# Kernel optimization log

Hardware: AMD Instinct MI355X
Metric: run time of the kernel (lower is better)

## Reference

```python
import jax, jax.numpy as jnp
import numpy as np

B, T, H, K = 128, 32, 256, 32


def setup_inputs() -> dict:
    key = jax.random.key(0)
    ks = jax.random.split(key, 24)
    s = 0.02  # small weight scale keeps exp(pdf) stable

    def n(k, shape, scale=s):
        return jax.random.normal(k, shape, dtype=jnp.float32) * scale

    inp = {
        "input_encoded": jax.random.normal(ks[0], (B, T, H), dtype=jnp.float32),
        "y_prev": jax.random.normal(ks[1], (B, T), dtype=jnp.float32),
        "attn_W1": n(ks[2], (H, 3 * H)),
        "attn_b1": n(ks[3], (H,)),
        "attn_W2": n(ks[4], (1, H)),
        "attn_b2": n(ks[5], (1,)),
        "fc_W": n(ks[6], (1, H + 1)),
        "fc_b": n(ks[7], (1,)),
        "var_W": n(ks[8], (H, H + 1)),
        "var_b": n(ks[9], (H,)),
        "W_ih": n(ks[10], (4 * H, 1)),
        "W_hh": n(ks[11], (4 * H, H)),
        "b_ih": n(ks[12], (4 * H,)),
        "b_hh": n(ks[13], (4 * H,)),
        "fc_dec_W": n(ks[14], (1, H)),
        "fc_dec_b": n(ks[15], (1,)),
        "pdf_W": n(ks[16], (1, H + 1)),
        "pdf_b": n(ks[17], (1,)),
        "fc_enc_W": n(ks[18], (1, H)),
        "fc_enc_b": n(ks[19], (1,)),
        "num_particles": K,
    }
    return inp


def reference(input_encoded, y_prev, attn_W1, attn_b1, attn_W2, attn_b2,
              fc_W, fc_b, var_W, var_b, W_ih, W_hh, b_ih, b_hh,
              fc_dec_W, fc_dec_b, pdf_W, pdf_b, fc_enc_W, fc_enc_b,
              num_particles):
    Bn, Tn, Hn = input_encoded.shape
    Kn = num_particles
    base = jax.random.key(42)
    arB = jnp.arange(Bn)

    def step(carry, xs):
        hiddens, cells = carry  # each (K*B, H), flat index = k*B + b
        t, y_t = xs  # y_t: (B,)
        k1, k2 = jax.random.split(jax.random.fold_in(base, t))
        # particle means (torch: mean over dim 0 of (K, B, H) view)
        hm = hiddens.reshape(Kn, Bn, Hn).mean(axis=0)  # (B, H)
        cm = cells.reshape(Kn, Bn, Hn).mean(axis=0)
        # attention over encoder timesteps
        x = jnp.concatenate([
            jnp.broadcast_to(hm[:, None, :], (Bn, Tn, Hn)),
            jnp.broadcast_to(cm[:, None, :], (Bn, Tn, Hn)),
            input_encoded], axis=2)  # (B, T, 3H)
        a = jnp.tanh(x @ attn_W1.T + attn_b1) @ attn_W2.T + attn_b2  # (B, T, 1)
        beta = jax.nn.softmax(a[..., 0], axis=1)  # (B, T)
        context = jnp.einsum('bt,bth->bh', beta, input_encoded)  # (B, H)
        y_tilde = jnp.concatenate([context, y_t[:, None]], axis=1) @ fc_W.T + fc_b  # (B, 1)
        var = jnp.concatenate([y_tilde, hm], axis=1) @ var_W.T + var_b  # (B, H)
        # single-step LSTM cell over all particles (torch gate order i,f,g,o)
        x_in = jnp.tile(y_tilde, (Kn, 1))  # (K*B, 1)
        gates = x_in @ W_ih.T + b_ih + hiddens @ W_hh.T + b_hh  # (K*B, 4H)
        i, f, g, o = jnp.split(gates, 4, axis=1)
        c_new = jax.nn.sigmoid(f) * cells + jax.nn.sigmoid(i) * jnp.tanh(g)
        h_new = jax.nn.sigmoid(o) * jnp.tanh(c_new)
        # reparameterization: h = mu + eps * softplus(var)
        std = jnp.tile(jax.nn.softplus(var), (Kn, 1))  # (K*B, H)
        eps = jax.random.normal(k1, (Kn * Bn, Hn), dtype=h_new.dtype)
        h_new = h_new + eps * std
        # sort_hidden: per-batch argsort of 1-d projection, gather hiddens only
        proj = h_new @ fc_dec_W.T + fc_dec_b  # (K*B, 1)
        idx = jnp.argsort(proj.reshape(Kn, Bn).T, axis=1)  # (B, K)
        flat = (arB[:, None] + idx * Bn).T.reshape(-1)  # (K*B,)
        h_sorted = h_new[flat]
        # particle weights (replicates torch's view(-1, K, 1) reshape exactly)
        y = jnp.concatenate([h_sorted, jnp.tile(y_tilde, (Kn, 1))], axis=1)
        prob = jnp.exp(y @ pdf_W.T + pdf_b).reshape(Bn, Kn, 1)
        prob = prob / prob.sum(axis=1, keepdims=True)
        # soft-resampling: multinomial over (B, K) rows (torch: prob.view(K,-1).T)
        logits = jnp.log(prob.reshape(Kn, Bn).T)  # (B, K)
        samp = jax.random.categorical(k2, logits, shape=(Kn, Bn))  # (K, B)
        flat2 = (samp * Bn + arB[None, :]).reshape(-1)
        return (h_sorted[flat2], c_new[flat2]), context

    h0 = jnp.zeros((Kn * Bn, Hn), dtype=input_encoded.dtype)
    (hiddens, _), contexts = jax.lax.scan(step, (h0, h0), (jnp.arange(Tn), y_prev.T))
    context = contexts[-1]
    hm = hiddens.reshape(Kn, Bn, Hn).mean(axis=0)  # (B, H)
    y_pred = hm @ fc_dec_W.T + fc_dec_b + context @ fc_enc_W.T + fc_enc_b  # (B, 1)
    return y_pred
```

## Files before the change

### kernel.cpp

```cpp
#include <hip/hip_runtime.h>
#include <cstdint>


#define Bn 128
#define Tn 32
#define Hn 256
#define Kn 32

__host__ __device__ inline void tf2x32(uint32_t k0, uint32_t k1, uint32_t x0, uint32_t x1,
                                       uint32_t &o0, uint32_t &o1) {
  uint32_t ks2 = k0 ^ k1 ^ 0x1BD11BDAu;
  x0 += k0; x1 += k1;
#define TFR(r) { x0 += x1; x1 = (x1 << r) | (x1 >> (32 - r)); x1 ^= x0; }
  TFR(13) TFR(15) TFR(26) TFR(6)
  x0 += k1;  x1 += ks2 + 1u;
  TFR(17) TFR(29) TFR(16) TFR(24)
  x0 += ks2; x1 += k0 + 2u;
  TFR(13) TFR(15) TFR(26) TFR(6)
  x0 += k0;  x1 += k1 + 3u;
  TFR(17) TFR(29) TFR(16) TFR(24)
  x0 += k1;  x1 += ks2 + 4u;
  TFR(13) TFR(15) TFR(26) TFR(6)
  x0 += ks2; x1 += k0 + 5u;
#undef TFR
  o0 = x0; o1 = x1;
}

__device__ __forceinline__ float erfinv_xla(float x) {
  float w = -log1pf(-x * x);
  float p;
  if (w < 5.0f) {
    w = w - 2.5f;
    p = 2.81022636e-08f;
    p = fmaf(p, w, 3.43273939e-07f);
    p = fmaf(p, w, -3.5233877e-06f);
    p = fmaf(p, w, -4.39150654e-06f);
    p = fmaf(p, w, 0.00021858087f);
    p = fmaf(p, w, -0.00125372503f);
    p = fmaf(p, w, -0.00417768164f);
    p = fmaf(p, w, 0.246640727f);
    p = fmaf(p, w, 1.50140941f);
  } else {
    w = sqrtf(w) - 3.0f;
    p = -0.000200214257f;
    p = fmaf(p, w, 0.000100950558f);
    p = fmaf(p, w, 0.00134934322f);
    p = fmaf(p, w, -0.00367342844f);
    p = fmaf(p, w, 0.00573950773f);
    p = fmaf(p, w, -0.0076224613f);
    p = fmaf(p, w, 0.00943887047f);
    p = fmaf(p, w, 1.00167406f);
    p = fmaf(p, w, 2.83297682f);
  }
  return p * x;
}

__device__ __forceinline__ float sigmoid_xla(float x) {
  return 0.5f + 0.5f * tanhf(0.5f * x);
}

__device__ __forceinline__ float u01_from_bits(uint32_t bits) {
  return __uint_as_float((bits >> 9) | 0x3F800000u) - 1.0f;
}

__device__ __forceinline__ float normal_from_idx(uint32_t ka, uint32_t kb, uint32_t idx) {
  uint32_t o0, o1; tf2x32(ka, kb, 0u, idx, o0, o1);
  float f = u01_from_bits(o0 ^ o1);
  const float LO = __uint_as_float(0xBF7FFFFFu);
  float u = fmaxf(LO, f * 2.0f + LO);
  return __uint_as_float(0x3FB504F3u) * erfinv_xla(u);
}

__device__ __forceinline__ float gumbel_from_idx(uint32_t ka, uint32_t kb, uint32_t idx) {
  uint32_t o0, o1; tf2x32(ka, kb, 0u, idx, o0, o1);
  float f = u01_from_bits(o0 ^ o1);
  const float TINY = __uint_as_float(0x00800000u);
  float u = fmaxf(TINY, f + TINY);
  return -logf(-logf(u));
}


__global__ void darnn_p0(const float* __restrict__ W1, const float* __restrict__ Whh,
                         const float* __restrict__ varW,
                         float* __restrict__ W1hT, float* __restrict__ W1cT,
                         float* __restrict__ W1eT, float* __restrict__ WhhT,
                         float* __restrict__ varWT) {
  int bid = blockIdx.x, tid = threadIdx.x;
  if (bid < 768) {
    int part = bid >> 8, j = bid & 255;
    float v = W1[tid * 768 + part * 256 + j];
    float* dst = (part == 0) ? W1hT : (part == 1) ? W1cT : W1eT;
    dst[j * 256 + tid] = v;
  } else if (bid < 1024) {
    int j = bid - 768;
    for (int idx = tid; idx < 1024; idx += 256) {
      int h = idx >> 2, q = idx & 3;
      WhhT[j * 1024 + idx] = Whh[(q * 256 + h) * 256 + j];
    }
  } else {
    int j2 = bid - 1024;
    varWT[j2 * 256 + tid] = varW[tid * 257 + j2];
  }
}

__global__ void darnn_p1(const float* __restrict__ enc, const float* __restrict__ W1eT,
                         const float* __restrict__ b1, float* __restrict__ encW1) {
  int bt = blockIdx.x, tid = threadIdx.x;
  __shared__ float se[256];
  se[tid] = enc[bt * 256 + tid];
  __syncthreads();
  float acc = 0.f;
  for (int j = 0; j < 256; ++j) acc = fmaf(se[j], W1eT[j * 256 + tid], acc);
  encW1[bt * 256 + tid] = acc + b1[tid];
}


__launch_bounds__(1024, 4)
__global__ void darnn_step(const float* __restrict__ enc, const float* __restrict__ yprev,
                           const float* __restrict__ W1hT, const float* __restrict__ W1cT,
                           const float* __restrict__ encW1, const float* __restrict__ W2,
                           const float* __restrict__ b2p, const float* __restrict__ fcW,
                           const float* __restrict__ fcbp, const float* __restrict__ varWT,
                           const float* __restrict__ varb, const float* __restrict__ WhhT,
                           const float* __restrict__ Wih, const float* __restrict__ bih,
                           const float* __restrict__ bhh, const float* __restrict__ decW,
                           const float* __restrict__ decbp, const float* __restrict__ pdfW,
                           const float* __restrict__ pdfbp,
                           const float* __restrict__ proj_p, const float* __restrict__ pdot_p,
                           const float* __restrict__ ytl_p,
                           const float* __restrict__ hprev, const float* __restrict__ cprev,
                           float* __restrict__ hcur, float* __restrict__ ccur,
                           float* __restrict__ proj_c, float* __restrict__ pdot_c,
                           float* __restrict__ ytl_c, float* __restrict__ ctx_g,
                           int t, uint32_t k1a, uint32_t k1b, uint32_t k2a, uint32_t k2b) {
  const int bid = blockIdx.x, tid = threadIdx.x;
  const int b = bid & 127, khalf = bid >> 7;
  const int bg = b >> 5, bloc = b & 31;
  const int h = tid & 255, kg = tid >> 8, lane = tid & 63;

  __shared__ __align__(16) float s_h[32 * 256];
  __shared__ float s_gp[1024], s_w[1024];
  __shared__ int s_srck[1024];
  __shared__ float s_ytlp[32], s_den[32], s_logit[32];
  __shared__ int s_rowH[32], s_rowC[32];
  __shared__ float s_hm[256], s_cm[256], s_hmc[256], s_red[256], s_std[256];
  __shared__ float s_sc[32], s_beta[32];
  __shared__ float s_ytl;
  __shared__ float s_sredP[16 * 4], s_sredQ[16 * 4];

  if (t > 0) {
    if (tid < 32) s_ytlp[tid] = ytl_p[bg * 32 + tid];
    {
      int bl = tid >> 5, k = tid & 31;
      s_gp[tid] = proj_p[k * 128 + bg * 32 + bl];
    }
    __syncthreads();
    {
      int bl = tid >> 5, k = tid & 31;
      float p = s_gp[tid];
      const float* gp = s_gp + bl * 32;
      int rank = 0;
      for (int kk = 0; kk < 32; ++kk) {
        float q = gp[kk];
        rank += (q < p) || (q == p && kk < k);
      }
      s_srck[bl * 32 + rank] = k;
      float wv = expf((pdot_p[k * 128 + bg * 32 + bl] + s_ytlp[bl] * pdfW[256]) + pdfbp[0]);
      s_w[bl * 32 + rank] = wv;
    }
    __syncthreads();
    if (tid < 32) {
      float s = 0.f;
      for (int bl = 0; bl < 32; ++bl) s += s_w[bl * 32 + tid];
      s_den[tid] = s;
    }
    __syncthreads();
    if (tid < 32) s_logit[tid] = logf(s_w[bloc * 32 + tid] / s_den[tid]);
    __syncthreads();
    if (tid < 32) {
      int ko = tid, r2 = ko * 128 + b;
      float best = gumbel_from_idx(k2a, k2b, (uint32_t)(r2 * 32)) + s_logit[0];
      int sv = 0;
      for (int k = 1; k < 32; ++k) {
        float v = gumbel_from_idx(k2a, k2b, (uint32_t)(r2 * 32 + k)) + s_logit[k];
        if (v > best) { best = v; sv = k; }
      }
      s_rowH[ko] = s_srck[bloc * 32 + sv] * 128 + b;
      s_rowC[ko] = sv * 128 + b;
    }
  } else {
    if (tid < 32) {
      s_rowH[tid] = tid * 128 + b;
      s_rowC[tid] = tid * 128 + b;
    }
  }
  __syncthreads();

  {
    const float4* hp = (const float4*)hprev;
    float4* sh4 = (float4*)s_h;
#pragma unroll
    for (int ii = 0; ii < 2; ++ii) {
      int i = tid + ii * 1024;
      int rr = i >> 6, c4 = i & 63;
      sh4[i] = hp[(size_t)s_rowH[rr] * 64 + c4];
    }
  }
  __syncthreads();

  if (tid < 256) {
    float s1 = 0.f;
    for (int k = 0; k < 32; ++k) s1 += s_h[k * 256 + tid];
    s_hm[tid] = s1 * 0.03125f;
  } else if (tid < 512) {
    int j = tid & 255;
    float s2 = 0.f;
    for (int k = 0; k < 32; ++k) s2 += cprev[(size_t)s_rowC[k] * 256 + j];
    s_cm[j] = s2 * 0.03125f;
  }
  __syncthreads();
  if (tid < 256) {
    float acc = 0.f;
    for (int j = 0; j < 256; ++j) {
      acc = fmaf(s_hm[j], W1hT[j * 256 + tid], acc);
      acc = fmaf(s_cm[j], W1cT[j * 256 + tid], acc);
    }
    s_hmc[tid] = acc;
  }
  __syncthreads();
  {
    int wv = tid >> 6;
    for (int tt = wv * 2; tt < wv * 2 + 2; ++tt) {
      float p = 0.f;
      for (int hh = lane; hh < 256; hh += 64)
        p += tanhf(encW1[(b * 32 + tt) * 256 + hh] + s_hmc[hh]) * W2[hh];
      for (int off = 32; off; off >>= 1) p += __shfl_down(p, off);
      if (lane == 0) s_sc[tt] = p + b2p[0];
    }
  }
  __syncthreads();
  if (tid == 0) {
    float m = s_sc[0];
    for (int k = 1; k < 32; ++k) m = fmaxf(m, s_sc[k]);
    float s = 0.f;
    for (int k = 0; k < 32; ++k) { float e = expf(s_sc[k] - m); s_beta[k] = e; s += e; }
    for (int k = 0; k < 32; ++k) s_beta[k] /= s;
  }
  __syncthreads();
  if (tid < 256) {
    float cx = 0.f;
    for (int tt = 0; tt < 32; ++tt) cx = fmaf(s_beta[tt], enc[(b * 32 + tt) * 256 + tid], cx);
    if (khalf == 0) ctx_g[b * 256 + tid] = cx;
    s_red[tid] = cx * fcW[tid];
  }
  __syncthreads();
  if (tid == 0) {
    float s = 0.f;
    for (int j = 0; j < 256; ++j) s += s_red[j];
    s += yprev[b * 32 + t] * fcW[256];
    s_ytl = s + fcbp[0];
    if (khalf == 0) ytl_c[b] = s_ytl;
  }
  __syncthreads();
  if (tid < 256) {
    float v = s_ytl * varWT[tid];
    for (int j = 0; j < 256; ++j) v = fmaf(s_hm[j], varWT[(1 + j) * 256 + tid], v);
    v += varb[tid];
    s_std[tid] = fmaxf(v, 0.f) + log1pf(expf(-fabsf(v)));
  }
  __syncthreads();

  float ai[4], af[4], ag[4], ao[4];
#pragma unroll
  for (int r = 0; r < 4; ++r) { ai[r] = af[r] = ag[r] = ao[r] = 0.f; }
  {
    const float4* wp = (const float4*)WhhT + h;
    const float* shr = s_h + (khalf * 16 + kg * 4) * 256;
    float4 wa0 = wp[0 * 256], wa1 = wp[1 * 256], wa2 = wp[2 * 256], wa3 = wp[3 * 256];
    for (int j = 0; j < 256; j += 4) {
      int jn = (j + 4) & 255;
      float4 wb0 = wp[(jn + 0) * 256];
      float4 wb1 = wp[(jn + 1) * 256];
      float4 wb2 = wp[(jn + 2) * 256];
      float4 wb3 = wp[(jn + 3) * 256];
#pragma unroll
      for (int r = 0; r < 4; ++r) {
        float4 h4 = *(const float4*)(shr + r * 256 + j);
        ai[r] = fmaf(h4.x, wa0.x, ai[r]); ai[r] = fmaf(h4.y, wa1.x, ai[r]);
        ai[r] = fmaf(h4.z, wa2.x, ai[r]); ai[r] = fmaf(h4.w, wa3.x, ai[r]);
        af[r] = fmaf(h4.x, wa0.y, af[r]); af[r] = fmaf(h4.y, wa1.y, af[r]);
        af[r] = fmaf(h4.z, wa2.y, af[r]); af[r] = fmaf(h4.w, wa3.y, af[r]);
        ag[r] = fmaf(h4.x, wa0.z, ag[r]); ag[r] = fmaf(h4.y, wa1.z, ag[r]);
        ag[r] = fmaf(h4.z, wa2.z, ag[r]); ag[r] = fmaf(h4.w, wa3.z, ag[r]);
        ao[r] = fmaf(h4.x, wa0.w, ao[r]); ao[r] = fmaf(h4.y, wa1.w, ao[r]);
        ao[r] = fmaf(h4.z, wa2.w, ao[r]); ao[r] = fmaf(h4.w, wa3.w, ao[r]);
      }
      wa0 = wb0; wa1 = wb1; wa2 = wb2; wa3 = wb3;
    }
  }

  const float bI = bih[h], bF = bih[256 + h], bG = bih[512 + h], bO = bih[768 + h];
  const float dI = bhh[h], dF = bhh[256 + h], dG = bhh[512 + h], dO = bhh[768 + h];
  const float wI = Wih[h], wF = Wih[256 + h], wG = Wih[512 + h], wO = Wih[768 + h];
  float hnv[4];
#pragma unroll
  for (int r = 0; r < 4; ++r) {
    int rl = kg * 4 + r;
    int k = khalf * 16 + rl, R = k * 128 + b;
    float xb = s_ytl;
    float pi = ((xb * wI + bI) + ai[r]) + dI;
    float pf = ((xb * wF + bF) + af[r]) + dF;
    float pg = ((xb * wG + bG) + ag[r]) + dG;
    float po = ((xb * wO + bO) + ao[r]) + dO;
    float c_old = cprev[(size_t)s_rowC[k] * 256 + h];
    float cn = sigmoid_xla(pf) * c_old + sigmoid_xla(pi) * tanhf(pg);
    float hn = sigmoid_xla(po) * tanhf(cn);
    float eps = normal_from_idx(k1a, k1b, (uint32_t)(R * 256 + h));
    hn = hn + eps * s_std[h];
    ccur[(size_t)R * 256 + h] = cn;
    hcur[(size_t)R * 256 + h] = hn;
    hnv[r] = hn;
  }

  const float dw = decW[h], pw = pdfW[h];
#pragma unroll
  for (int r = 0; r < 4; ++r) {
    int rl = kg * 4 + r;
    float v = hnv[r] * dw;
    for (int off = 32; off; off >>= 1) v += __shfl_down(v, off);
    if (lane == 0) s_sredP[rl * 4 + (h >> 6)] = v;
    float v2 = hnv[r] * pw;
    for (int off = 32; off; off >>= 1) v2 += __shfl_down(v2, off);
    if (lane == 0) s_sredQ[rl * 4 + (h >> 6)] = v2;
  }
  __syncthreads();
  if (tid < 16) {
    int rl = tid, k = khalf * 16 + rl;
    proj_c[k * 128 + b] = ((s_sredP[rl * 4 + 0] + s_sredP[rl * 4 + 1]) +
                           (s_sredP[rl * 4 + 2] + s_sredP[rl * 4 + 3])) + decbp[0];
  } else if (tid < 32) {
    int rl = tid - 16, k = khalf * 16 + rl;
    pdot_c[k * 128 + b] = (s_sredQ[rl * 4 + 0] + s_sredQ[rl * 4 + 1]) +
                          (s_sredQ[rl * 4 + 2] + s_sredQ[rl * 4 + 3]);
  }
}


__launch_bounds__(256)
__global__ void darnn_kout(const float* __restrict__ proj_g, const float* __restrict__ pdot_g,
                           const float* __restrict__ ytl_prev, const float* __restrict__ hprev,
                           const float* __restrict__ ctx_g, const float* __restrict__ decW,
                           const float* __restrict__ decbp, const float* __restrict__ encWo,
                           const float* __restrict__ encbo, const float* __restrict__ pdfW,
                           const float* __restrict__ pdfbp,
                           uint32_t k2a, uint32_t k2b, float* __restrict__ out) {
  const int b = blockIdx.x, tid = threadIdx.x, bg = b >> 5, bloc = b & 31;
  const int lane = tid & 63;
  __shared__ float s_gp[1024], s_w[1024];
  __shared__ int s_srck[1024];
  __shared__ float s_ytlp[32], s_den[32], s_logit[32];
  __shared__ int s_row[32];
  __shared__ float s_hm[256], s_sred[8];

  if (tid < 32) s_ytlp[tid] = ytl_prev[bg * 32 + tid];
  for (int i = tid; i < 1024; i += 256) {
    int bl = i >> 5, k = i & 31;
    s_gp[i] = proj_g[k * 128 + bg * 32 + bl];
  }
  __syncthreads();
  for (int i = tid; i < 1024; i += 256) {
    int bl = i >> 5, k = i & 31;
    float p = s_gp[i];
    const float* gp = s_gp + bl * 32;
    int rank = 0;
    for (int kk = 0; kk < 32; ++kk) {
      float q = gp[kk];
      rank += (q < p) || (q == p && kk < k);
    }
    s_srck[bl * 32 + rank] = k;
    float wv = expf((pdot_g[k * 128 + bg * 32 + bl] + s_ytlp[bl] * pdfW[256]) + pdfbp[0]);
    s_w[bl * 32 + rank] = wv;
  }
  __syncthreads();
  if (tid < 32) {
    float s = 0.f;
    for (int bl = 0; bl < 32; ++bl) s += s_w[bl * 32 + tid];
    s_den[tid] = s;
  }
  __syncthreads();
  if (tid < 32) s_logit[tid] = logf(s_w[bloc * 32 + tid] / s_den[tid]);
  __syncthreads();
  if (tid < 32) {
    int ko = tid, r2 = ko * 128 + b;
    float best = gumbel_from_idx(k2a, k2b, (uint32_t)(r2 * 32)) + s_logit[0];
    int sv = 0;
    for (int k = 1; k < 32; ++k) {
      float v = gumbel_from_idx(k2a, k2b, (uint32_t)(r2 * 32 + k)) + s_logit[k];
      if (v > best) { best = v; sv = k; }
    }
    s_row[ko] = s_srck[bloc * 32 + sv] * 128 + b;
  }
  __syncthreads();
  {
    float s1 = 0.f;
    for (int k = 0; k < 32; ++k) s1 += hprev[(size_t)s_row[k] * 256 + tid];
    s_hm[tid] = s1 * 0.03125f;
  }
  __syncthreads();
  {
    int wvi = tid >> 6;
    float v1 = s_hm[tid] * decW[tid];
    float v2 = ctx_g[b * 256 + tid] * encWo[tid];
    for (int off = 32; off; off >>= 1) { v1 += __shfl_down(v1, off); v2 += __shfl_down(v2, off); }
    if (lane == 0) { s_sred[wvi] = v1; s_sred[4 + wvi] = v2; }
  }
  __syncthreads();
  if (tid == 0) {
    float d1 = (s_sred[0] + s_sred[1]) + (s_sred[2] + s_sred[3]);
    float d2 = (s_sred[4] + s_sred[5]) + (s_sred[6] + s_sred[7]);
    out[b] = ((d1 + decbp[0]) + d2) + encbo[0];
  }
}

extern "C" void kernel_launch(void* const* d_in, const int* in_sizes, int n_in,
                              void* d_out, int out_size, void* d_ws, size_t ws_size,
                              hipStream_t stream) {
  const float* enc   = (const float*)d_in[0];
  const float* yprev = (const float*)d_in[1];
  const float* W1    = (const float*)d_in[2];
  const float* b1    = (const float*)d_in[3];
  const float* W2    = (const float*)d_in[4];
  const float* b2    = (const float*)d_in[5];
  const float* fcW   = (const float*)d_in[6];
  const float* fcb   = (const float*)d_in[7];
  const float* varW  = (const float*)d_in[8];
  const float* varb  = (const float*)d_in[9];
  const float* Wih   = (const float*)d_in[10];
  const float* Whh   = (const float*)d_in[11];
  const float* bih   = (const float*)d_in[12];
  const float* bhh   = (const float*)d_in[13];
  const float* decW  = (const float*)d_in[14];
  const float* decb  = (const float*)d_in[15];
  const float* pdfW  = (const float*)d_in[16];
  const float* pdfb  = (const float*)d_in[17];
  const float* encWo = (const float*)d_in[18];
  const float* encbo = (const float*)d_in[19];

  float* ws = (float*)d_ws;
  size_t o = 0;
  float* encW1 = ws + o; o += (size_t)Bn * Tn * Hn;
  float* W1hT  = ws + o; o += (size_t)Hn * Hn;
  float* W1cT  = ws + o; o += (size_t)Hn * Hn;
  float* W1eT  = ws + o; o += (size_t)Hn * Hn;
  float* WhhT  = ws + o; o += (size_t)Hn * 4 * Hn;
  float* varWT = ws + o; o += (size_t)257 * Hn;
  float* hbuf0 = ws + o; o += (size_t)Kn * Bn * Hn;
  float* hbuf1 = ws + o; o += (size_t)Kn * Bn * Hn;
  float* cbuf0 = ws + o; o += (size_t)Kn * Bn * Hn;
  float* cbuf1 = ws + o; o += (size_t)Kn * Bn * Hn;
  float* ytl0  = ws + o; o += 128;
  float* ytl1  = ws + o; o += 128;
  float* ctx_g = ws + o; o += (size_t)Bn * Hn;
  float* proj0 = ws + o; o += 4096;
  float* proj1 = ws + o; o += 4096;
  float* pdot0 = ws + o; o += 4096;
  float* pdot1 = ws + o; o += 4096;
  if (ws_size < o * sizeof(float)) return;

  float* hb[2] = { hbuf0, hbuf1 };
  float* cb[2] = { cbuf0, cbuf1 };
  float* yb[2] = { ytl0, ytl1 };
  float* pp[2] = { proj0, proj1 };
  float* pq[2] = { pdot0, pdot1 };

  hipMemsetAsync(hbuf1, 0, (size_t)Kn * Bn * Hn * sizeof(float), stream);
  hipMemsetAsync(cbuf1, 0, (size_t)Kn * Bn * Hn * sizeof(float), stream);

  darnn_p0<<<1281, 256, 0, stream>>>(W1, Whh, varW, W1hT, W1cT, W1eT, WhhT, varWT);
  darnn_p1<<<Bn * Tn, 256, 0, stream>>>(enc, W1eT, b1, encW1);

  uint32_t k2pa = 0, k2pb = 0;
  for (int t = 0; t < Tn; ++t) {
    uint32_t f0, f1, k1a, k1b, k2a, k2b;
    tf2x32(0u, 42u, 0u, (uint32_t)t, f0, f1);
    tf2x32(f0, f1, 0u, 0u, k1a, k1b);
    tf2x32(f0, f1, 0u, 1u, k2a, k2b);
    int cur = t & 1, prv = (t + 1) & 1;

    darnn_step<<<2 * Bn, 1024, 0, stream>>>(enc, yprev, W1hT, W1cT, encW1, W2, b2,
                                            fcW, fcb, varWT, varb, WhhT, Wih, bih, bhh,
                                            decW, decb, pdfW, pdfb,
                                            pp[prv], pq[prv], yb[prv], hb[prv], cb[prv],
                                            hb[cur], cb[cur], pp[cur], pq[cur], yb[cur],
                                            ctx_g, t, k1a, k1b, k2pa, k2pb);
    k2pa = k2a; k2pb = k2b;
  }

  darnn_kout<<<Bn, 256, 0, stream>>>(pp[1], pq[1], yb[1], hb[1], ctx_g,
                                     decW, decb, encWo, encbo, pdfW, pdfb,
                                     k2pa, k2pb, (float*)d_out);
}
```

Measured before the change: 2.866 ms.

## Split particles across four blocks per batch and parallelize Gumbel sampling

The recurrent step kernel now launches four blocks per batch element instead of two, with each block handling 8 particles. This shrinks the shared hidden-state tile and the per-thread gate accumulators, which raises occupancy and parallelism. Gumbel noise for the resampling step is now computed by all 1024 threads into shared memory instead of 32 threads looping serially. The mean and matvec loops are unrolled to batch their global loads, and the first half of the threads computes the means while the rest stage the hidden tile. The cost is that every block repeats the per-batch attention and projection prologue, so that redundant work doubles.

```diff
diff --git a/kernel.cpp b/kernel.cpp
--- a/kernel.cpp
+++ b/kernel.cpp
@@ -115,7 +115,7 @@
 }
 
 
-__launch_bounds__(1024, 4)
+__launch_bounds__(1024, 8)
 __global__ void darnn_step(const float* __restrict__ enc, const float* __restrict__ yprev,
                            const float* __restrict__ W1hT, const float* __restrict__ W1cT,
                            const float* __restrict__ encW1, const float* __restrict__ W2,
@@ -138,15 +138,15 @@
   const int bg = b >> 5, bloc = b & 31;
   const int h = tid & 255, kg = tid >> 8, lane = tid & 63;
 
-  __shared__ __align__(16) float s_h[32 * 256];
-  __shared__ float s_gp[1024], s_w[1024];
+  __shared__ __align__(16) float s_h[8 * 256];
+  __shared__ float s_gp[1024], s_w[1024], s_gvals[1024];
   __shared__ int s_srck[1024];
   __shared__ float s_ytlp[32], s_den[32], s_logit[32];
   __shared__ int s_rowH[32], s_rowC[32];
-  __shared__ float s_hm[256], s_cm[256], s_hmc[256], s_red[256], s_std[256];
+  __shared__ __align__(16) float s_hm[256], s_cm[256], s_hmc[256], s_red[256], s_std[256];
   __shared__ float s_sc[32], s_beta[32];
   __shared__ float s_ytl;
-  __shared__ float s_sredP[16 * 4], s_sredQ[16 * 4];
+  __shared__ float s_sredP[8 * 4], s_sredQ[8 * 4];
 
   if (t > 0) {
     if (tid < 32) s_ytlp[tid] = ytl_p[bg * 32 + tid];
@@ -177,14 +177,17 @@
     __syncthreads();
     if (tid < 32) s_logit[tid] = logf(s_w[bloc * 32 + tid] / s_den[tid]);
     __syncthreads();
+    {
+      int ko = tid >> 5, k = tid & 31, r2 = ko * 128 + b;
+      s_gvals[tid] = gumbel_from_idx(k2a, k2b, (uint32_t)(r2 * 32 + k)) + s_logit[k];
+    }
+    __syncthreads();
     if (tid < 32) {
-      int ko = tid, r2 = ko * 128 + b;
-      float best = gumbel_from_idx(k2a, k2b, (uint32_t)(r2 * 32)) + s_logit[0];
+      int ko = tid;
+      const float* gv = s_gvals + ko * 32;
+      float best = gv[0];
       int sv = 0;
-      for (int k = 1; k < 32; ++k) {
-        float v = gumbel_from_idx(k2a, k2b, (uint32_t)(r2 * 32 + k)) + s_logit[k];
-        if (v > best) { best = v; sv = k; }
-      }
+      for (int k = 1; k < 32; ++k) { float v = gv[k]; if (v > best) { best = v; sv = k; } }
       s_rowH[ko] = s_srck[bloc * 32 + sv] * 128 + b;
       s_rowC[ko] = sv * 128 + b;
     }
@@ -196,38 +199,53 @@
   }
   __syncthreads();
 
-  {
-    const float4* hp = (const float4*)hprev;
-    float4* sh4 = (float4*)s_h;
-#pragma unroll
-    for (int ii = 0; ii < 2; ++ii) {
-      int i = tid + ii * 1024;
-      int rr = i >> 6, c4 = i & 63;
-      sh4[i] = hp[(size_t)s_rowH[rr] * 64 + c4];
-    }
-  }
-  __syncthreads();
-
   if (tid < 256) {
     float s1 = 0.f;
-    for (int k = 0; k < 32; ++k) s1 += s_h[k * 256 + tid];
+    for (int k0 = 0; k0 < 32; k0 += 8) {
+      float hv[8];
+#pragma unroll
+      for (int i = 0; i < 8; ++i) hv[i] = hprev[(size_t)s_rowH[k0 + i] * 256 + tid];
+#pragma unroll
+      for (int i = 0; i < 8; ++i) s1 += hv[i];
+    }
     s_hm[tid] = s1 * 0.03125f;
   } else if (tid < 512) {
     int j = tid & 255;
     float s2 = 0.f;
-    for (int k = 0; k < 32; ++k) s2 += cprev[(size_t)s_rowC[k] * 256 + j];
+    for (int k0 = 0; k0 < 32; k0 += 8) {
+      float cv[8];
+#pragma unroll
+      for (int i = 0; i < 8; ++i) cv[i] = cprev[(size_t)s_rowC[k0 + i] * 256 + j];
+#pragma unroll
+      for (int i = 0; i < 8; ++i) s2 += cv[i];
+    }
     s_cm[j] = s2 * 0.03125f;
-  }
-  __syncthreads();
+  } else {
+    int i = tid - 512;
+    int rr = i >> 6, c4 = i & 63;
+    ((float4*)s_h)[i] = ((const float4*)hprev)[(size_t)s_rowH[khalf * 8 + rr] * 64 + c4];
+  }
+  __syncthreads();
+
   if (tid < 256) {
     float acc = 0.f;
-    for (int j = 0; j < 256; ++j) {
-      acc = fmaf(s_hm[j], W1hT[j * 256 + tid], acc);
-      acc = fmaf(s_cm[j], W1cT[j * 256 + tid], acc);
+    for (int j0 = 0; j0 < 256; j0 += 8) {
+      float wh[8], wc[8];
+#pragma unroll
+      for (int i = 0; i < 8; ++i) {
+        wh[i] = W1hT[(j0 + i) * 256 + tid];
+        wc[i] = W1cT[(j0 + i) * 256 + tid];
+      }
+#pragma unroll
+      for (int i = 0; i < 8; ++i) {
+        acc = fmaf(s_hm[j0 + i], wh[i], acc);
+        acc = fmaf(s_cm[j0 + i], wc[i], acc);
+      }
     }
     s_hmc[tid] = acc;
   }
   __syncthreads();
+
   {
     int wv = tid >> 6;
     for (int tt = wv * 2; tt < wv * 2 + 2; ++tt) {
@@ -255,8 +273,12 @@
   }
   __syncthreads();
   if (tid == 0) {
+    const float4* r4 = (const float4*)s_red;
     float s = 0.f;
-    for (int j = 0; j < 256; ++j) s += s_red[j];
+    for (int i = 0; i < 64; ++i) {
+      float4 v = r4[i];
+      s = s + v.x; s = s + v.y; s = s + v.z; s = s + v.w;
+    }
     s += yprev[b * 32 + t] * fcW[256];
     s_ytl = s + fcbp[0];
     if (khalf == 0) ytl_c[b] = s_ytl;
@@ -264,49 +286,52 @@
   __syncthreads();
   if (tid < 256) {
     float v = s_ytl * varWT[tid];
-    for (int j = 0; j < 256; ++j) v = fmaf(s_hm[j], varWT[(1 + j) * 256 + tid], v);
+    for (int j0 = 0; j0 < 256; j0 += 16) {
+      float wv[16];
+#pragma unroll
+      for (int i = 0; i < 16; ++i) wv[i] = varWT[(1 + j0 + i) * 256 + tid];
+#pragma unroll
+      for (int i = 0; i < 16; ++i) v = fmaf(s_hm[j0 + i], wv[i], v);
+    }
     v += varb[tid];
     s_std[tid] = fmaxf(v, 0.f) + log1pf(expf(-fabsf(v)));
   }
   __syncthreads();
 
-  float ai[4], af[4], ag[4], ao[4];
-#pragma unroll
-  for (int r = 0; r < 4; ++r) { ai[r] = af[r] = ag[r] = ao[r] = 0.f; }
+  float ai[2], af[2], ag[2], ao[2];
+#pragma unroll
+  for (int r = 0; r < 2; ++r) { ai[r] = af[r] = ag[r] = ao[r] = 0.f; }
   {
     const float4* wp = (const float4*)WhhT + h;
-    const float* shr = s_h + (khalf * 16 + kg * 4) * 256;
-    float4 wa0 = wp[0 * 256], wa1 = wp[1 * 256], wa2 = wp[2 * 256], wa3 = wp[3 * 256];
+    const float* shr = s_h + (kg * 2) * 256;
     for (int j = 0; j < 256; j += 4) {
-      int jn = (j + 4) & 255;
-      float4 wb0 = wp[(jn + 0) * 256];
-      float4 wb1 = wp[(jn + 1) * 256];
-      float4 wb2 = wp[(jn + 2) * 256];
-      float4 wb3 = wp[(jn + 3) * 256];
-#pragma unroll
-      for (int r = 0; r < 4; ++r) {
+      float4 w0 = wp[(j + 0) * 256];
+      float4 w1 = wp[(j + 1) * 256];
+      float4 w2 = wp[(j + 2) * 256];
+      float4 w3 = wp[(j + 3) * 256];
+#pragma unroll
+      for (int r = 0; r < 2; ++r) {
         float4 h4 = *(const float4*)(shr + r * 256 + j);
-        ai[r] = fmaf(h4.x, wa0.x, ai[r]); ai[r] = fmaf(h4.y, wa1.x, ai[r]);
-        ai[r] = fmaf(h4.z, wa2.x, ai[r]); ai[r] = fmaf(h4.w, wa3.x, ai[r]);
-        af[r] = fmaf(h4.x, wa0.y, af[r]); af[r] = fmaf(h4.y, wa1.y, af[r]);
-        af[r] = fmaf(h4.z, wa2.y, af[r]); af[r] = fmaf(h4.w, wa3.y, af[r]);
-        ag[r] = fmaf(h4.x, wa0.z, ag[r]); ag[r] = fmaf(h4.y, wa1.z, ag[r]);
-        ag[r] = fmaf(h4.z, wa2.z, ag[r]); ag[r] = fmaf(h4.w, wa3.z, ag[r]);
-        ao[r] = fmaf(h4.x, wa0.w, ao[r]); ao[r] = fmaf(h4.y, wa1.w, ao[r]);
-        ao[r] = fmaf(h4.z, wa2.w, ao[r]); ao[r] = fmaf(h4.w, wa3.w, ao[r]);
+        ai[r] = fmaf(h4.x, w0.x, ai[r]); ai[r] = fmaf(h4.y, w1.x, ai[r]);
+        ai[r] = fmaf(h4.z, w2.x, ai[r]); ai[r] = fmaf(h4.w, w3.x, ai[r]);
+        af[r] = fmaf(h4.x, w0.y, af[r]); af[r] = fmaf(h4.y, w1.y, af[r]);
+        af[r] = fmaf(h4.z, w2.y, af[r]); af[r] = fmaf(h4.w, w3.y, af[r]);
+        ag[r] = fmaf(h4.x, w0.z, ag[r]); ag[r] = fmaf(h4.y, w1.z, ag[r]);
+        ag[r] = fmaf(h4.z, w2.z, ag[r]); ag[r] = fmaf(h4.w, w3.z, ag[r]);
+        ao[r] = fmaf(h4.x, w0.w, ao[r]); ao[r] = fmaf(h4.y, w1.w, ao[r]);
+        ao[r] = fmaf(h4.z, w2.w, ao[r]); ao[r] = fmaf(h4.w, w3.w, ao[r]);
       }
-      wa0 = wb0; wa1 = wb1; wa2 = wb2; wa3 = wb3;
     }
   }
 
   const float bI = bih[h], bF = bih[256 + h], bG = bih[512 + h], bO = bih[768 + h];
   const float dI = bhh[h], dF = bhh[256 + h], dG = bhh[512 + h], dO = bhh[768 + h];
   const float wI = Wih[h], wF = Wih[256 + h], wG = Wih[512 + h], wO = Wih[768 + h];
-  float hnv[4];
-#pragma unroll
-  for (int r = 0; r < 4; ++r) {
-    int rl = kg * 4 + r;
-    int k = khalf * 16 + rl, R = k * 128 + b;
+  float hnv[2];
+#pragma unroll
+  for (int r = 0; r < 2; ++r) {
+    int rl = kg * 2 + r;
+    int k = khalf * 8 + rl, R = k * 128 + b;
     float xb = s_ytl;
     float pi = ((xb * wI + bI) + ai[r]) + dI;
     float pf = ((xb * wF + bF) + af[r]) + dF;
@@ -324,8 +349,8 @@
 
   const float dw = decW[h], pw = pdfW[h];
 #pragma unroll
-  for (int r = 0; r < 4; ++r) {
-    int rl = kg * 4 + r;
+  for (int r = 0; r < 2; ++r) {
+    int rl = kg * 2 + r;
     float v = hnv[r] * dw;
     for (int off = 32; off; off >>= 1) v += __shfl_down(v, off);
     if (lane == 0) s_sredP[rl * 4 + (h >> 6)] = v;
@@ -334,12 +359,12 @@
     if (lane == 0) s_sredQ[rl * 4 + (h >> 6)] = v2;
   }
   __syncthreads();
-  if (tid < 16) {
-    int rl = tid, k = khalf * 16 + rl;
+  if (tid < 8) {
+    int rl = tid, k = khalf * 8 + rl;
     proj_c[k * 128 + b] = ((s_sredP[rl * 4 + 0] + s_sredP[rl * 4 + 1]) +
                            (s_sredP[rl * 4 + 2] + s_sredP[rl * 4 + 3])) + decbp[0];
-  } else if (tid < 32) {
-    int rl = tid - 16, k = khalf * 16 + rl;
+  } else if (tid < 16) {
+    int rl = tid - 8, k = khalf * 8 + rl;
     pdot_c[k * 128 + b] = (s_sredQ[rl * 4 + 0] + s_sredQ[rl * 4 + 1]) +
                           (s_sredQ[rl * 4 + 2] + s_sredQ[rl * 4 + 3]);
   }
@@ -487,7 +512,7 @@
     tf2x32(f0, f1, 0u, 1u, k2a, k2b);
     int cur = t & 1, prv = (t + 1) & 1;
 
-    darnn_step<<<2 * Bn, 1024, 0, stream>>>(enc, yprev, W1hT, W1cT, encW1, W2, b2,
+    darnn_step<<<4 * Bn, 1024, 0, stream>>>(enc, yprev, W1hT, W1cT, encW1, W2, b2,
                                             fcW, fcb, varWT, varb, WhhT, Wih, bih, bhh,
                                             decW, decb, pdfW, pdfb,
                                             pp[prv], pq[prv], yb[prv], hb[prv], cb[prv],
```

Result: slower. 3.530 ms (+23.2%).
